# Kernel tuning notes

Measured on AMD Instinct MI355X. Metric: run time of the kernel, lower is better.

The kernel has to match this reference:

```python
import jax, jax.numpy as jnp
import numpy as np

N_NODES = 50000
N_EDGES = 1600000
IN_CH = 128
HEADS = 4
OUT_PER_HEAD = 32  # out_channels // heads with concat=True
NEG_SLOPE = 0.2    # GATConv default leaky_relu slope
SOFTMAX_EPS = 1e-16  # PyG scatter-softmax denominator eps
LN_EPS = 1e-5


def setup_inputs() -> dict:
    key = jax.random.key(0)
    ks = jax.random.split(key, 8)
    x = jax.random.normal(ks[0], (N_NODES, IN_CH), dtype=jnp.float32)
    edge_index = jax.random.randint(ks[1], (2, N_EDGES), 0, N_NODES, dtype=jnp.int32)
    W = jax.random.normal(ks[2], (IN_CH, HEADS * OUT_PER_HEAD), dtype=jnp.float32) * (1.0 / np.sqrt(IN_CH))
    att_src = jax.random.normal(ks[3], (HEADS, OUT_PER_HEAD), dtype=jnp.float32) * 0.1
    att_dst = jax.random.normal(ks[4], (HEADS, OUT_PER_HEAD), dtype=jnp.float32) * 0.1
    bias = jnp.zeros((HEADS * OUT_PER_HEAD,), dtype=jnp.float32)
    gamma = jnp.ones((HEADS * OUT_PER_HEAD,), dtype=jnp.float32)
    beta = jnp.zeros((HEADS * OUT_PER_HEAD,), dtype=jnp.float32)
    return {"x": x, "edge_index": edge_index, "W": W, "att_src": att_src,
            "att_dst": att_dst, "bias": bias, "gamma": gamma, "beta": beta}


def reference(x, edge_index, W, att_src, att_dst, bias, gamma, beta):
    N = x.shape[0]
    H, C = att_src.shape
    # GATConv default add_self_loops=True
    loop = jnp.arange(N, dtype=edge_index.dtype)
    src = jnp.concatenate([edge_index[0], loop])  # message source j
    dst = jnp.concatenate([edge_index[1], loop])  # aggregation target i

    h = (x @ W).reshape(N, H, C)                      # [N,H,C]
    a_s = jnp.einsum('nhc,hc->nh', h, att_src)        # [N,H]
    a_d = jnp.einsum('nhc,hc->nh', h, att_dst)        # [N,H]

    logits = jax.nn.leaky_relu(a_s[src] + a_d[dst], NEG_SLOPE)  # [E,H]
    # segment softmax over edges grouped by destination node
    m = jax.ops.segment_max(logits, dst, num_segments=N)        # [N,H]
    m = jnp.where(jnp.isfinite(m), m, 0.0)
    e = jnp.exp(logits - m[dst])
    s = jax.ops.segment_sum(e, dst, num_segments=N)             # [N,H]
    alpha = e / (s[dst] + SOFTMAX_EPS)                          # [E,H]

    msg = h[src] * alpha[:, :, None]                            # [E,H,C]
    out = jax.ops.segment_sum(msg, dst, num_segments=N)         # [N,H,C]
    out = out.reshape(N, H * C) + bias

    mu = out.mean(axis=-1, keepdims=True)
    var = ((out - mu) ** 2).mean(axis=-1, keepdims=True)
    y = (out - mu) / jnp.sqrt(var + LN_EPS) * gamma + beta
    return jax.nn.elu(y)
```

## Files before the change

kernel.cpp:

```cpp
#include <hip/hip_runtime.h>
#include <hip/hip_bf16.h>
#include <hip/hip_fp16.h>

typedef __hip_bfloat16 bf16;
typedef unsigned int u32;
typedef unsigned short u16;
typedef unsigned long long u64;

constexpr int N   = 50000;
constexpr int E   = 1600000;
constexpr int C   = 128;
constexpr int H   = 4;
constexpr int NB  = 782;
constexpr int CAP = 2560;
constexpr int CHUNK = 4096;
constexpr float NEG  = 0.2f;
constexpr float SEPS = 1e-16f;
constexpr float LEPS = 1e-5f;

__device__ __forceinline__ float lo16(u32 v) { return __uint_as_float(v << 16); }
__device__ __forceinline__ float hi16(u32 v) { return __uint_as_float(v & 0xFFFF0000u); }

__global__ __launch_bounds__(256) void k1_gemm(
    const float* __restrict__ x, const float* __restrict__ W,
    const float* __restrict__ att_s, const float* __restrict__ att_d,
    bf16* __restrict__ hb, float* __restrict__ as_, float* __restrict__ ad_)
{
    const int nb = blockIdx.x * 16;
    const int t  = threadIdx.x;
    __shared__ float sx[16 * 128];
    const float4* xg = (const float4*)(x + nb * 128);
    ((float4*)sx)[t]       = xg[t];
    ((float4*)sx)[t + 256] = xg[t + 256];
    __syncthreads();

    const int c = t & 127;
    const int g = t >> 7;
    const float* xb = sx + (g << 10);
    float acc[8] = {0.f, 0.f, 0.f, 0.f, 0.f, 0.f, 0.f, 0.f};

    for (int k = 0; k < 128; k += 4) {
        const float w0 = W[(k + 0) * 128 + c];
        const float w1 = W[(k + 1) * 128 + c];
        const float w2 = W[(k + 2) * 128 + c];
        const float w3 = W[(k + 3) * 128 + c];
#pragma unroll
        for (int j = 0; j < 8; ++j) {
            const float4 xv = *(const float4*)(xb + j * 128 + k);
            acc[j] = fmaf(xv.x, w0, fmaf(xv.y, w1, fmaf(xv.z, w2, fmaf(xv.w, w3, acc[j]))));
        }
    }

    const int lane = t & 63;
    const int head = c >> 5;
    const float asc = att_s[c], adc = att_d[c];
#pragma unroll
    for (int j = 0; j < 8; ++j) {
        const int node = nb + (g << 3) + j;
        hb[node * 128 + c] = __float2bfloat16(acc[j]);
        float vs = acc[j] * asc;
        float vd = acc[j] * adc;
#pragma unroll
        for (int off = 16; off; off >>= 1) {
            vs += __shfl_xor(vs, off, 64);
            vd += __shfl_xor(vd, off, 64);
        }
        if ((lane & 31) == 0) {
            as_[node * H + head] = vs;
            ad_[node * H + head] = vd;
        }
    }
}

__global__ __launch_bounds__(256) void kbin(
    const int* __restrict__ ei, u32* __restrict__ gcur, u32* __restrict__ pairs)
{
    __shared__ u32 lcnt[NB], lbase[NB], lfill[NB];
    __shared__ u16 dstl[CHUNK];
    const int t = threadIdx.x;
    const int base = blockIdx.x * CHUNK;
    const int nE = min(CHUNK, E - base);
    for (int i = t; i < NB; i += 256) lcnt[i] = 0;
    __syncthreads();
    for (int i = t; i < nE; i += 256) {
        u32 d = (u32)ei[E + base + i];
        dstl[i] = (u16)d;
        atomicAdd(&lcnt[d >> 6], 1u);
    }
    __syncthreads();
    for (int i = t; i < NB; i += 256) {
        u32 cb = lcnt[i];
        lbase[i] = cb ? atomicAdd(&gcur[i], cb) : 0u;
        lfill[i] = 0u;
    }
    __syncthreads();
    for (int i = t; i < nE; i += 256) {
        u32 src = (u32)ei[base + i];
        u32 dst = (u32)dstl[i];
        u32 b = dst >> 6;
        u32 pos = atomicAdd(&lfill[b], 1u);
        pairs[(size_t)b * CAP + lbase[b] + pos] = src | ((dst & 63u) << 16);
    }
}

__global__ __launch_bounds__(256) void kfill2(
    const u32* __restrict__ pairs, const u32* __restrict__ gcur,
    const float4* __restrict__ as4, const float4* __restrict__ ad4,
    int* __restrict__ row_ptr, u16* __restrict__ col, __half* __restrict__ whf)
{
    __shared__ int jcnt[64], joff[64], jcur[64];
    __shared__ float4 adl[64];
    __shared__ u32 ssum[4];
    const int b = blockIdx.x, t = threadIdx.x;
    const int wave = t >> 6, lane = t & 63;
    const int cntb = (int)gcur[b];

    u32 part = 0;
    for (int i = t; i < b; i += 256) part += gcur[i];
#pragma unroll
    for (int off = 32; off; off >>= 1) part += __shfl_xor(part, off, 64);
    if (lane == 0) ssum[wave] = part;
    if (t < 64) {
        jcnt[t] = 0;
        const int n = b * 64 + t;
        adl[t] = (n < N) ? ad4[n] : make_float4(0.f, 0.f, 0.f, 0.f);
    }
    if (b == 0 && t == 255) row_ptr[N] = E;
    __syncthreads();
    const int base = (int)(ssum[0] + ssum[1] + ssum[2] + ssum[3]);

    const u32* pr = pairs + (size_t)b * CAP;
    for (int i = t; i < cntb; i += 256) atomicAdd(&jcnt[pr[i] >> 16], 1);
    __syncthreads();
    if (t < 64) {
        int v = jcnt[t], incl = v;
#pragma unroll
        for (int off = 1; off < 64; off <<= 1) {
            int u = __shfl_up(incl, off, 64);
            if (t >= off) incl += u;
        }
        joff[t] = incl - v;
        const int n = b * 64 + t;
        if (n < N) row_ptr[n] = base + joff[t];
        jcur[t] = 0;
    }
    __syncthreads();
    for (int i = t; i < cntb; i += 256) {
        const u32 p = pr[i];
        const int j = p >> 16;
        const u32 s = p & 0xFFFFu;
        const int pos = atomicAdd(&jcur[j], 1);
        const int idx = base + joff[j] + pos;
        col[idx] = (u16)s;
        const float4 a = as4[s];
        const float4 d = adl[j];
        float l0 = a.x + d.x, l1 = a.y + d.y, l2 = a.z + d.z, l3 = a.w + d.w;
        l0 = fmaxf(l0, NEG * l0); l1 = fmaxf(l1, NEG * l1);
        l2 = fmaxf(l2, NEG * l2); l3 = fmaxf(l3, NEG * l3);
        __half2 w01; w01.x = __float2half(__expf(l0)); w01.y = __float2half(__expf(l1));
        __half2 w23; w23.x = __float2half(__expf(l2)); w23.y = __float2half(__expf(l3));
        *(__half2*)(whf + (size_t)idx * 4)     = w01;
        *(__half2*)(whf + (size_t)idx * 4 + 2) = w23;
    }
}

__global__ __launch_bounds__(256) void kd_agg_ln(
    const int* __restrict__ row_ptr, const u16* __restrict__ col,
    const __half* __restrict__ whf, const u32* __restrict__ hb,
    const float* __restrict__ as_, const float* __restrict__ ad_,
    const float* __restrict__ bias, const float* __restrict__ gamma,
    const float* __restrict__ beta, float* __restrict__ out)
{
    int gid = blockIdx.x * blockDim.x + threadIdx.x;
    int n = gid >> 6;
    if (n >= N) return;
    const int lane = gid & 63;
    const int head = lane >> 4;

    float l = as_[n * H + head] + ad_[n * H + head];
    l = fmaxf(l, NEG * l);
    float w = __expf(l);
    float den = w;
    u32 hv = hb[n * 64 + lane];
    float num0 = w * lo16(hv);
    float num1 = w * hi16(hv);

    int k = row_ptr[n];
    const int end = row_ptr[n + 1];
    for (; k + 8 <= end; k += 8) {
        int   s[8]; float ww[8]; u32 v[8];
#pragma unroll
        for (int i = 0; i < 8; ++i) s[i] = col[k + i];
#pragma unroll
        for (int i = 0; i < 8; ++i) ww[i] = __half2float(whf[(size_t)(k + i) * 4 + head]);
#pragma unroll
        for (int i = 0; i < 8; ++i) v[i] = hb[s[i] * 64 + lane];
#pragma unroll
        for (int i = 0; i < 8; ++i) {
            den += ww[i];
            num0 = fmaf(ww[i], lo16(v[i]), num0);
            num1 = fmaf(ww[i], hi16(v[i]), num1);
        }
    }
    for (; k < end; ++k) {
        const int s = col[k];
        const float ws = __half2float(whf[(size_t)k * 4 + head]);
        const u32 vs = hb[s * 64 + lane];
        den += ws;
        num0 = fmaf(ws, lo16(vs), num0);
        num1 = fmaf(ws, hi16(vs), num1);
    }

    const int c0 = lane * 2;
    const float inv_den = 1.f / (den + SEPS);
    float v0 = num0 * inv_den + bias[c0];
    float v1 = num1 * inv_den + bias[c0 + 1];

    float sum = v0 + v1;
#pragma unroll
    for (int off = 32; off; off >>= 1) sum += __shfl_xor(sum, off, 64);
    const float mu = sum * (1.0f / C);
    const float d0 = v0 - mu, d1 = v1 - mu;
    float sq = d0 * d0 + d1 * d1;
#pragma unroll
    for (int off = 32; off; off >>= 1) sq += __shfl_xor(sq, off, 64);
    const float inv = rsqrtf(sq * (1.0f / C) + LEPS);
    float y0 = d0 * inv * gamma[c0]     + beta[c0];
    float y1 = d1 * inv * gamma[c0 + 1] + beta[c0 + 1];
    y0 = y0 > 0.f ? y0 : __expf(y0) - 1.f;
    y1 = y1 > 0.f ? y1 : __expf(y1) - 1.f;
    float2 o; o.x = y0; o.y = y1;
    *(float2*)(out + (size_t)n * C + c0) = o;
}

extern "C" void kernel_launch(void* const* d_in, const int* in_sizes, int n_in,
                              void* d_out, int out_size, void* d_ws, size_t ws_size,
                              hipStream_t stream)
{
    const float* x     = (const float*)d_in[0];
    const int*   ei    = (const int*)  d_in[1];
    const float* W     = (const float*)d_in[2];
    const float* att_s = (const float*)d_in[3];
    const float* att_d = (const float*)d_in[4];
    const float* bias  = (const float*)d_in[5];
    const float* gamma = (const float*)d_in[6];
    const float* beta  = (const float*)d_in[7];
    float* out = (float*)d_out;

    char* p = (char*)d_ws;
    bf16*   hb      = (bf16*)p;   p += (size_t)N * C * sizeof(bf16);
    float*  as_     = (float*)p;  p += (size_t)N * H * sizeof(float);
    float*  ad_     = (float*)p;  p += (size_t)N * H * sizeof(float);
    u32*    pairs   = (u32*)p;    p += (size_t)NB * CAP * sizeof(u32);
    u16*    col     = (u16*)p;    p += ((size_t)E * sizeof(u16) + 15) & ~(size_t)15;
    __half* whf     = (__half*)p; p += (size_t)E * 4 * sizeof(__half);
    int*    row_ptr = (int*)p;    p += ((size_t)(N + 1) * sizeof(int) + 15) & ~(size_t)15;
    u32*    gcur    = (u32*)p;

    hipMemsetAsync(gcur, 0, NB * sizeof(u32), stream);
    k1_gemm<<<N / 16, 256, 0, stream>>>(x, W, att_s, att_d, hb, as_, ad_);
    kbin<<<(E + CHUNK - 1) / CHUNK, 256, 0, stream>>>(ei, gcur, pairs);
    kfill2<<<NB, 256, 0, stream>>>(pairs, gcur, (const float4*)as_,
                                   (const float4*)ad_, row_ptr, col, whf);
    kd_agg_ln<<<(N * 64) / 256, 256, 0, stream>>>(
        row_ptr, col, whf, (const u32*)hb, as_, ad_, bias, gamma, beta, out);
}
```

Before: 245.8 us.

## Retile GEMM, shrink bin chunks, transpose edge weights per head, vectorize gather loads

The GEMM now processes 32 nodes per block, with each thread computing a 4x4 register tile through float4 weight loads. The edge-weight array changes from interleaved [E,4] to head-major [4,E], so the aggregation loop can read eight consecutive weights and column indices with vector loads after an alignment peel. The binning chunk shrinks to 1024 edges for more blocks, and kfill2 runs 512 threads per block. The goal is fewer memory instructions and less uncoalesced traffic in the gather, and more parallelism in the preprocessing kernels. The cost is scattered 2-byte stores per head in kfill2 and more global atomics on the bin cursors.

```diff
diff --git a/kernel.cpp b/kernel.cpp
--- a/kernel.cpp
+++ b/kernel.cpp
@@ -5,7 +5,6 @@
 typedef __hip_bfloat16 bf16;
 typedef unsigned int u32;
 typedef unsigned short u16;
-typedef unsigned long long u64;
 
 constexpr int N   = 50000;
 constexpr int E   = 1600000;
@@ -13,7 +12,7 @@
 constexpr int H   = 4;
 constexpr int NB  = 782;
 constexpr int CAP = 2560;
-constexpr int CHUNK = 4096;
+constexpr int CHUNK = 1024;
 constexpr float NEG  = 0.2f;
 constexpr float SEPS = 1e-16f;
 constexpr float LEPS = 1e-5f;
@@ -26,46 +25,63 @@
     const float* __restrict__ att_s, const float* __restrict__ att_d,
     bf16* __restrict__ hb, float* __restrict__ as_, float* __restrict__ ad_)
 {
-    const int nb = blockIdx.x * 16;
+    const int nb = blockIdx.x * 32;
     const int t  = threadIdx.x;
-    __shared__ float sx[16 * 128];
-    const float4* xg = (const float4*)(x + nb * 128);
-    ((float4*)sx)[t]       = xg[t];
-    ((float4*)sx)[t + 256] = xg[t + 256];
-    __syncthreads();
-
-    const int c = t & 127;
-    const int g = t >> 7;
-    const float* xb = sx + (g << 10);
-    float acc[8] = {0.f, 0.f, 0.f, 0.f, 0.f, 0.f, 0.f, 0.f};
+    __shared__ float sx[32 * 128];
+    const float4* xg = (const float4*)(x + (size_t)nb * 128);
+    const int maxv = min(32, N - nb) * 32;
+#pragma unroll
+    for (int i = 0; i < 4; ++i) {
+        int idx = t + i * 256;
+        ((float4*)sx)[idx] = (idx < maxv) ? xg[idx] : make_float4(0.f, 0.f, 0.f, 0.f);
+    }
+    __syncthreads();
+
+    const int cg = t & 31;
+    const int c0 = cg * 4;
+    const int g  = t >> 5;
+    const float* xb = sx + g * 4 * 128;
+    float4 acc[4];
+#pragma unroll
+    for (int j = 0; j < 4; ++j) acc[j] = make_float4(0.f, 0.f, 0.f, 0.f);
 
     for (int k = 0; k < 128; k += 4) {
-        const float w0 = W[(k + 0) * 128 + c];
-        const float w1 = W[(k + 1) * 128 + c];
-        const float w2 = W[(k + 2) * 128 + c];
-        const float w3 = W[(k + 3) * 128 + c];
-#pragma unroll
-        for (int j = 0; j < 8; ++j) {
+        const float4 w0 = *(const float4*)(W + (size_t)(k + 0) * 128 + c0);
+        const float4 w1 = *(const float4*)(W + (size_t)(k + 1) * 128 + c0);
+        const float4 w2 = *(const float4*)(W + (size_t)(k + 2) * 128 + c0);
+        const float4 w3 = *(const float4*)(W + (size_t)(k + 3) * 128 + c0);
+#pragma unroll
+        for (int j = 0; j < 4; ++j) {
             const float4 xv = *(const float4*)(xb + j * 128 + k);
-            acc[j] = fmaf(xv.x, w0, fmaf(xv.y, w1, fmaf(xv.z, w2, fmaf(xv.w, w3, acc[j]))));
-        }
-    }
-
-    const int lane = t & 63;
-    const int head = c >> 5;
-    const float asc = att_s[c], adc = att_d[c];
-#pragma unroll
-    for (int j = 0; j < 8; ++j) {
-        const int node = nb + (g << 3) + j;
-        hb[node * 128 + c] = __float2bfloat16(acc[j]);
-        float vs = acc[j] * asc;
-        float vd = acc[j] * adc;
-#pragma unroll
-        for (int off = 16; off; off >>= 1) {
+            acc[j].x = fmaf(xv.x, w0.x, fmaf(xv.y, w1.x, fmaf(xv.z, w2.x, fmaf(xv.w, w3.x, acc[j].x))));
+            acc[j].y = fmaf(xv.x, w0.y, fmaf(xv.y, w1.y, fmaf(xv.z, w2.y, fmaf(xv.w, w3.y, acc[j].y))));
+            acc[j].z = fmaf(xv.x, w0.z, fmaf(xv.y, w1.z, fmaf(xv.z, w2.z, fmaf(xv.w, w3.z, acc[j].z))));
+            acc[j].w = fmaf(xv.x, w0.w, fmaf(xv.y, w1.w, fmaf(xv.z, w2.w, fmaf(xv.w, w3.w, acc[j].w))));
+        }
+    }
+
+    const float4 asv = *(const float4*)(att_s + c0);
+    const float4 adv = *(const float4*)(att_d + c0);
+    const int head = cg >> 3;
+#pragma unroll
+    for (int j = 0; j < 4; ++j) {
+        const int node = nb + g * 4 + j;
+        const bool valid = node < N;
+        if (valid) {
+            __hip_bfloat162 p01, p23;
+            p01.x = __float2bfloat16(acc[j].x); p01.y = __float2bfloat16(acc[j].y);
+            p23.x = __float2bfloat16(acc[j].z); p23.y = __float2bfloat16(acc[j].w);
+            *(__hip_bfloat162*)(hb + (size_t)node * 128 + c0)     = p01;
+            *(__hip_bfloat162*)(hb + (size_t)node * 128 + c0 + 2) = p23;
+        }
+        float vs = acc[j].x * asv.x + acc[j].y * asv.y + acc[j].z * asv.z + acc[j].w * asv.w;
+        float vd = acc[j].x * adv.x + acc[j].y * adv.y + acc[j].z * adv.z + acc[j].w * adv.w;
+#pragma unroll
+        for (int off = 1; off < 8; off <<= 1) {
             vs += __shfl_xor(vs, off, 64);
             vd += __shfl_xor(vd, off, 64);
         }
-        if ((lane & 31) == 0) {
+        if (valid && ((cg & 7) == 0)) {
             as_[node * H + head] = vs;
             ad_[node * H + head] = vd;
         }
@@ -103,20 +119,20 @@
     }
 }
 
-__global__ __launch_bounds__(256) void kfill2(
+__global__ __launch_bounds__(512) void kfill2(
     const u32* __restrict__ pairs, const u32* __restrict__ gcur,
     const float4* __restrict__ as4, const float4* __restrict__ ad4,
-    int* __restrict__ row_ptr, u16* __restrict__ col, __half* __restrict__ whf)
+    int* __restrict__ row_ptr, u16* __restrict__ col, u16* __restrict__ whf)
 {
     __shared__ int jcnt[64], joff[64], jcur[64];
     __shared__ float4 adl[64];
-    __shared__ u32 ssum[4];
+    __shared__ u32 ssum[8];
     const int b = blockIdx.x, t = threadIdx.x;
     const int wave = t >> 6, lane = t & 63;
     const int cntb = (int)gcur[b];
 
     u32 part = 0;
-    for (int i = t; i < b; i += 256) part += gcur[i];
+    for (int i = t; i < b; i += 512) part += gcur[i];
 #pragma unroll
     for (int off = 32; off; off >>= 1) part += __shfl_xor(part, off, 64);
     if (lane == 0) ssum[wave] = part;
@@ -125,12 +141,13 @@
         const int n = b * 64 + t;
         adl[t] = (n < N) ? ad4[n] : make_float4(0.f, 0.f, 0.f, 0.f);
     }
-    if (b == 0 && t == 255) row_ptr[N] = E;
-    __syncthreads();
-    const int base = (int)(ssum[0] + ssum[1] + ssum[2] + ssum[3]);
+    if (b == 0 && t == 511) row_ptr[N] = E;
+    __syncthreads();
+    const int base = (int)(ssum[0] + ssum[1] + ssum[2] + ssum[3] +
+                           ssum[4] + ssum[5] + ssum[6] + ssum[7]);
 
     const u32* pr = pairs + (size_t)b * CAP;
-    for (int i = t; i < cntb; i += 256) atomicAdd(&jcnt[pr[i] >> 16], 1);
+    for (int i = t; i < cntb; i += 512) atomicAdd(&jcnt[pr[i] >> 16], 1);
     __syncthreads();
     if (t < 64) {
         int v = jcnt[t], incl = v;
@@ -145,7 +162,7 @@
         jcur[t] = 0;
     }
     __syncthreads();
-    for (int i = t; i < cntb; i += 256) {
+    for (int i = t; i < cntb; i += 512) {
         const u32 p = pr[i];
         const int j = p >> 16;
         const u32 s = p & 0xFFFFu;
@@ -157,16 +174,20 @@
         float l0 = a.x + d.x, l1 = a.y + d.y, l2 = a.z + d.z, l3 = a.w + d.w;
         l0 = fmaxf(l0, NEG * l0); l1 = fmaxf(l1, NEG * l1);
         l2 = fmaxf(l2, NEG * l2); l3 = fmaxf(l3, NEG * l3);
-        __half2 w01; w01.x = __float2half(__expf(l0)); w01.y = __float2half(__expf(l1));
-        __half2 w23; w23.x = __float2half(__expf(l2)); w23.y = __float2half(__expf(l3));
-        *(__half2*)(whf + (size_t)idx * 4)     = w01;
-        *(__half2*)(whf + (size_t)idx * 4 + 2) = w23;
+        __half h0 = __float2half(__expf(l0));
+        __half h1 = __float2half(__expf(l1));
+        __half h2 = __float2half(__expf(l2));
+        __half h3 = __float2half(__expf(l3));
+        whf[0 * (size_t)E + idx] = __half_as_ushort(h0);
+        whf[1 * (size_t)E + idx] = __half_as_ushort(h1);
+        whf[2 * (size_t)E + idx] = __half_as_ushort(h2);
+        whf[3 * (size_t)E + idx] = __half_as_ushort(h3);
     }
 }
 
 __global__ __launch_bounds__(256) void kd_agg_ln(
     const int* __restrict__ row_ptr, const u16* __restrict__ col,
-    const __half* __restrict__ whf, const u32* __restrict__ hb,
+    const u16* __restrict__ whf, const u32* __restrict__ hb,
     const float* __restrict__ as_, const float* __restrict__ ad_,
     const float* __restrict__ bias, const float* __restrict__ gamma,
     const float* __restrict__ beta, float* __restrict__ out)
@@ -176,6 +197,7 @@
     if (n >= N) return;
     const int lane = gid & 63;
     const int head = lane >> 4;
+    const u16* whh = whf + (size_t)head * E;
 
     float l = as_[n * H + head] + ad_[n * H + head];
     l = fmaxf(l, NEG * l);
@@ -187,24 +209,49 @@
 
     int k = row_ptr[n];
     const int end = row_ptr[n + 1];
+    if ((k & 1) && k < end) {
+        const int s = col[k];
+        const float ws = __half2float(__ushort_as_half(whh[k]));
+        const u32 vs = hb[s * 64 + lane];
+        den += ws;
+        num0 = fmaf(ws, lo16(vs), num0);
+        num1 = fmaf(ws, hi16(vs), num1);
+        ++k;
+    }
     for (; k + 8 <= end; k += 8) {
-        int   s[8]; float ww[8]; u32 v[8];
-#pragma unroll
-        for (int i = 0; i < 8; ++i) s[i] = col[k + i];
-#pragma unroll
-        for (int i = 0; i < 8; ++i) ww[i] = __half2float(whf[(size_t)(k + i) * 4 + head]);
-#pragma unroll
-        for (int i = 0; i < 8; ++i) v[i] = hb[s[i] * 64 + lane];
-#pragma unroll
-        for (int i = 0; i < 8; ++i) {
-            den += ww[i];
-            num0 = fmaf(ww[i], lo16(v[i]), num0);
-            num1 = fmaf(ww[i], hi16(v[i]), num1);
-        }
+        const uint2 ca = *(const uint2*)(col + k);
+        const uint2 cb = *(const uint2*)(col + k + 4);
+        const uint2 wa = *(const uint2*)(whh + k);
+        const uint2 wb = *(const uint2*)(whh + k + 4);
+        const int s0 = ca.x & 0xFFFF, s1 = ca.x >> 16;
+        const int s2 = ca.y & 0xFFFF, s3 = ca.y >> 16;
+        const int s4 = cb.x & 0xFFFF, s5 = cb.x >> 16;
+        const int s6 = cb.y & 0xFFFF, s7 = cb.y >> 16;
+        const u32 v0 = hb[s0 * 64 + lane], v1 = hb[s1 * 64 + lane];
+        const u32 v2 = hb[s2 * 64 + lane], v3 = hb[s3 * 64 + lane];
+        const u32 v4 = hb[s4 * 64 + lane], v5 = hb[s5 * 64 + lane];
+        const u32 v6 = hb[s6 * 64 + lane], v7 = hb[s7 * 64 + lane];
+        const float w0 = __half2float(__ushort_as_half((u16)(wa.x & 0xFFFF)));
+        const float w1 = __half2float(__ushort_as_half((u16)(wa.x >> 16)));
+        const float w2 = __half2float(__ushort_as_half((u16)(wa.y & 0xFFFF)));
+        const float w3 = __half2float(__ushort_as_half((u16)(wa.y >> 16)));
+        const float w4 = __half2float(__ushort_as_half((u16)(wb.x & 0xFFFF)));
+        const float w5 = __half2float(__ushort_as_half((u16)(wb.x >> 16)));
+        const float w6 = __half2float(__ushort_as_half((u16)(wb.y & 0xFFFF)));
+        const float w7 = __half2float(__ushort_as_half((u16)(wb.y >> 16)));
+        den += ((w0 + w1) + (w2 + w3)) + ((w4 + w5) + (w6 + w7));
+        num0 = fmaf(w0, lo16(v0), num0); num1 = fmaf(w0, hi16(v0), num1);
+        num0 = fmaf(w1, lo16(v1), num0); num1 = fmaf(w1, hi16(v1), num1);
+        num0 = fmaf(w2, lo16(v2), num0); num1 = fmaf(w2, hi16(v2), num1);
+        num0 = fmaf(w3, lo16(v3), num0); num1 = fmaf(w3, hi16(v3), num1);
+        num0 = fmaf(w4, lo16(v4), num0); num1 = fmaf(w4, hi16(v4), num1);
+        num0 = fmaf(w5, lo16(v5), num0); num1 = fmaf(w5, hi16(v5), num1);
+        num0 = fmaf(w6, lo16(v6), num0); num1 = fmaf(w6, hi16(v6), num1);
+        num0 = fmaf(w7, lo16(v7), num0); num1 = fmaf(w7, hi16(v7), num1);
     }
     for (; k < end; ++k) {
         const int s = col[k];
-        const float ws = __half2float(whf[(size_t)k * 4 + head]);
+        const float ws = __half2float(__ushort_as_half(whh[k]));
         const u32 vs = hb[s * 64 + lane];
         den += ws;
         num0 = fmaf(ws, lo16(vs), num0);
@@ -248,19 +295,19 @@
     float* out = (float*)d_out;
 
     char* p = (char*)d_ws;
-    bf16*   hb      = (bf16*)p;   p += (size_t)N * C * sizeof(bf16);
-    float*  as_     = (float*)p;  p += (size_t)N * H * sizeof(float);
-    float*  ad_     = (float*)p;  p += (size_t)N * H * sizeof(float);
-    u32*    pairs   = (u32*)p;    p += (size_t)NB * CAP * sizeof(u32);
-    u16*    col     = (u16*)p;    p += ((size_t)E * sizeof(u16) + 15) & ~(size_t)15;
-    __half* whf     = (__half*)p; p += (size_t)E * 4 * sizeof(__half);
-    int*    row_ptr = (int*)p;    p += ((size_t)(N + 1) * sizeof(int) + 15) & ~(size_t)15;
-    u32*    gcur    = (u32*)p;
+    bf16*  hb      = (bf16*)p;   p += (size_t)N * C * sizeof(bf16);
+    float* as_     = (float*)p;  p += (size_t)N * H * sizeof(float);
+    float* ad_     = (float*)p;  p += (size_t)N * H * sizeof(float);
+    u32*   pairs   = (u32*)p;    p += (size_t)NB * CAP * sizeof(u32);
+    u16*   col     = (u16*)p;    p += ((size_t)E * sizeof(u16) + 15) & ~(size_t)15;
+    u16*   whf     = (u16*)p;    p += (size_t)E * 4 * sizeof(u16);
+    int*   row_ptr = (int*)p;    p += ((size_t)(N + 1) * sizeof(int) + 15) & ~(size_t)15;
+    u32*   gcur    = (u32*)p;
 
     hipMemsetAsync(gcur, 0, NB * sizeof(u32), stream);
-    k1_gemm<<<N / 16, 256, 0, stream>>>(x, W, att_s, att_d, hb, as_, ad_);
+    k1_gemm<<<(N + 31) / 32, 256, 0, stream>>>(x, W, att_s, att_d, hb, as_, ad_);
     kbin<<<(E + CHUNK - 1) / CHUNK, 256, 0, stream>>>(ei, gcur, pairs);
-    kfill2<<<NB, 256, 0, stream>>>(pairs, gcur, (const float4*)as_,
+    kfill2<<<NB, 512, 0, stream>>>(pairs, gcur, (const float4*)as_,
                                    (const float4*)ad_, row_ptr, col, whf);
     kd_agg_ln<<<(N * 64) / 256, 256, 0, stream>>>(
         row_ptr, col, whf, (const u32*)hb, as_, ad_, bias, gamma, beta, out);
```

Measured after the change: 306.6 us. 1.25x slower.
